# Kernel optimization log

Hardware: AMD Instinct MI355X
Metric: run time of the kernel (lower is better)

The kernel has to match this reference:

```python
import jax, jax.numpy as jnp
import numpy as np

T, B, D, H, O = 64, 64, 512, 512, 128

def setup_inputs() -> dict:
    key = jax.random.key(0)
    ks = jax.random.split(key, 8)
    s = 0.05
    return {
        "x": jax.random.normal(ks[0], (T, B, D), jnp.float32),
        "w_ih": jax.random.normal(ks[1], (T, 4 * H, D), jnp.float32) * s,
        "w_hh": jax.random.normal(ks[2], (T, 4 * H, H), jnp.float32) * s,
        "b_ih": jax.random.normal(ks[3], (T, 4 * H), jnp.float32) * s,
        "b_hh": jax.random.normal(ks[4], (T, 4 * H), jnp.float32) * s,
        "w_ho": jax.random.normal(ks[5], (O, H), jnp.float32) * s,
        "b_ho": jax.random.normal(ks[6], (O,), jnp.float32) * s,
        "lengths": jax.random.randint(ks[7], (B,), 1, T + 1, jnp.int64 if jax.config.jax_enable_x64 else jnp.int32),
    }

def _lstm_scan(x, w_ih, w_hh, b_ih, b_hh):
    bs = x.shape[1]
    h0 = jnp.zeros((bs, H), x.dtype)
    c0 = jnp.zeros((bs, H), x.dtype)

    def step(carry, inp):
        h, c = carry
        xt, Wih, Whh, bih, bhh = inp
        # gates: [B, 4H], torch gate order i, f, g, o
        gates = xt @ Wih.T + bih + h @ Whh.T + bhh
        i, f, g, o = jnp.split(gates, 4, axis=-1)
        c = jax.nn.sigmoid(f) * c + jax.nn.sigmoid(i) * jnp.tanh(g)
        h = jax.nn.sigmoid(o) * jnp.tanh(c)
        return (h, c), h

    (_, _), outs = jax.lax.scan(step, (h0, c0), (x, w_ih, w_hh, b_ih, b_hh))
    return outs  # [T, B, H]

def reference(x, w_ih, w_hh, b_ih, b_hh, w_ho, b_ho, lengths):
    outs = _lstm_scan(x, w_ih, w_hh, b_ih, b_hh)
    bs = x.shape[1]
    h_t = outs[lengths - 1, jnp.arange(bs)]  # [B, H] last valid output per seq
    logits = h_t @ w_ho.T + b_ho
    return jax.nn.log_softmax(logits, axis=1)
```

## Files before the change

### kernel.cpp

```cpp
#include <hip/hip_runtime.h>
#include <math.h>

#define TT 64
#define BB 64
#define DD 512
#define HH 512
#define G4 2048
#define OO 128

typedef unsigned short us16;
typedef __attribute__((ext_vector_type(8))) short bf16x8;
typedef __attribute__((ext_vector_type(4))) float f32x4;

__device__ __forceinline__ unsigned pk_bf16(float lo, float hi) {
  unsigned r;
  asm volatile("v_cvt_pk_bf16_f32 %0, %1, %2" : "=v"(r) : "v"(lo), "v"(hi));
  return r;
}

__device__ __forceinline__ float sigm(float v) { return 1.f / (1.f + expf(-v)); }

__device__ __forceinline__ uint4 load_b128_cc(const void* p) {
  uint4 r;
  asm volatile("global_load_dwordx4 %0, %1, off sc0 sc1" : "=v"(r) : "v"(p));
  return r;
}
__device__ __forceinline__ void store_b64_cc(void* p, uint2 v) {
  asm volatile("global_store_dwordx2 %0, %1, off sc0 sc1" ::"v"(p), "v"(v) : "memory");
}

__global__ __launch_bounds__(256) void phaseA_mfma(
    const float* __restrict__ x, const float* __restrict__ wih,
    const float* __restrict__ bih, const float* __restrict__ bhh,
    float* __restrict__ Gb) {
  __shared__ us16 xa[2][64][64];
  __shared__ us16 wbuf[2][128][64];
  const int tid = threadIdx.x;
  const int t = blockIdx.y;
  const int j0 = blockIdx.x * 128;
  const int wv = tid >> 6, lane = tid & 63;
  const int wm = wv & 1, wn = wv >> 1;
  const float* xb = x + (size_t)t * (BB * DD);
  const float* wg = wih + (size_t)t * (G4 * DD) + (size_t)j0 * DD;

  float4 xr[2][2], wr[4][2];
  int xrow[2], xc[2], wrow[4], wc[4];
#pragma unroll
  for (int i = 0; i < 2; i++) { int cid = tid + i * 256; xrow[i] = cid >> 3; xc[i] = cid & 7; }
#pragma unroll
  for (int i = 0; i < 4; i++) { int cid = tid + i * 256; wrow[i] = cid >> 3; wc[i] = cid & 7; }

  auto loadx = [&](int k0) {
#pragma unroll
    for (int i = 0; i < 2; i++) {
      const float* p = xb + xrow[i] * DD + k0 + xc[i] * 8;
      xr[i][0] = *(const float4*)p; xr[i][1] = *(const float4*)(p + 4);
    }
  };
  auto loadw = [&](int k0) {
#pragma unroll
    for (int i = 0; i < 4; i++) {
      const float* p = wg + (size_t)wrow[i] * DD + k0 + wc[i] * 8;
      wr[i][0] = *(const float4*)p; wr[i][1] = *(const float4*)(p + 4);
    }
  };
  auto store = [&](int buf) {
#pragma unroll
    for (int i = 0; i < 2; i++) {
      uint4 u;
      u.x = pk_bf16(xr[i][0].x, xr[i][0].y); u.y = pk_bf16(xr[i][0].z, xr[i][0].w);
      u.z = pk_bf16(xr[i][1].x, xr[i][1].y); u.w = pk_bf16(xr[i][1].z, xr[i][1].w);
      int p = xc[i] ^ (xrow[i] & 7);
      *(uint4*)&xa[buf][xrow[i]][p * 8] = u;
    }
#pragma unroll
    for (int i = 0; i < 4; i++) {
      uint4 u;
      u.x = pk_bf16(wr[i][0].x, wr[i][0].y); u.y = pk_bf16(wr[i][0].z, wr[i][0].w);
      u.z = pk_bf16(wr[i][1].x, wr[i][1].y); u.w = pk_bf16(wr[i][1].z, wr[i][1].w);
      int p = wc[i] ^ (wrow[i] & 7);
      *(uint4*)&wbuf[buf][wrow[i]][p * 8] = u;
    }
  };

  loadx(0); loadw(0); store(0);
  __syncthreads();

  f32x4 zero = {0.f, 0.f, 0.f, 0.f};
  f32x4 acc[2][4];
#pragma unroll
  for (int mt = 0; mt < 2; mt++)
#pragma unroll
    for (int nt = 0; nt < 4; nt++) acc[mt][nt] = zero;

  for (int s = 0; s < 8; s++) {
    const int nb = s & 1;
    if (s < 7) { loadx((s + 1) * 64); loadw((s + 1) * 64); }
#pragma unroll
    for (int ks = 0; ks < 2; ks++) {
      const int cc = ks * 4 + (lane >> 4);
      bf16x8 a[2], b[4];
#pragma unroll
      for (int mt = 0; mt < 2; mt++) {
        int r = wm * 32 + mt * 16 + (lane & 15);
        a[mt] = *(const bf16x8*)&xa[nb][r][(cc ^ (r & 7)) * 8];
      }
#pragma unroll
      for (int nt = 0; nt < 4; nt++) {
        int r = wn * 64 + nt * 16 + (lane & 15);
        b[nt] = *(const bf16x8*)&wbuf[nb][r][(cc ^ (r & 7)) * 8];
      }
#pragma unroll
      for (int mt = 0; mt < 2; mt++)
#pragma unroll
        for (int nt = 0; nt < 4; nt++)
          acc[mt][nt] = __builtin_amdgcn_mfma_f32_16x16x32_bf16(a[mt], b[nt], acc[mt][nt], 0, 0, 0);
    }
    __syncthreads();
    if (s < 7) store(nb ^ 1);
    __syncthreads();
  }

  float bias[4]; int jn[4];
#pragma unroll
  for (int nt = 0; nt < 4; nt++) {
    jn[nt] = j0 + wn * 64 + nt * 16 + (lane & 15);
    bias[nt] = bih[t * G4 + jn[nt]] + bhh[t * G4 + jn[nt]];
  }
#pragma unroll
  for (int mt = 0; mt < 2; mt++)
#pragma unroll
    for (int nt = 0; nt < 4; nt++)
#pragma unroll
      for (int e = 0; e < 4; e++) {
        int brow = wm * 32 + mt * 16 + (lane >> 4) * 4 + e;
        Gb[((size_t)t * BB + brow) * G4 + jn[nt]] = acc[mt][nt][e] + bias[nt];
      }
}

__global__ __launch_bounds__(256, 1) void lstm_persist(
    const float* __restrict__ whh, const float* __restrict__ Gb,
    const int* __restrict__ lengths, us16* __restrict__ hb,
    float* __restrict__ cbuf, float* __restrict__ hf,
    unsigned* __restrict__ flags) {
  __shared__ float gm[2][16][36];

  const int tid = threadIdx.x, bid = blockIdx.x;
  const int bh = bid & 1, ug = bid >> 1;
  const int wv = tid >> 6, lane = tid & 63;
  const int wm = wv & 1, kq = wv >> 1;
  const int l15 = lane & 15, klg = lane >> 4;

  const size_t jrow = (size_t)((l15 >> 2) * 512 + ug * 4 + (l15 & 3));

  float4 pf[8][2];
  auto prefW = [&](int tt) {
    const float* wt = whh + (size_t)tt * (G4 * HH) + jrow * HH;
#pragma unroll
    for (int s = 0; s < 8; s++) {
      const float* p = wt + (size_t)(kq * 32 + s * 4 + klg) * 8;
      pf[s][0] = *(const float4*)p;
      pf[s][1] = *(const float4*)(p + 4);
    }
  };
  bf16x8 wfrag[8];
  auto cvtW = [&]() {
#pragma unroll
    for (int s = 0; s < 8; s++) {
      uint4 u;
      u.x = pk_bf16(pf[s][0].x, pf[s][0].y); u.y = pk_bf16(pf[s][0].z, pf[s][0].w);
      u.z = pk_bf16(pf[s][1].x, pf[s][1].y); u.w = pk_bf16(pf[s][1].z, pf[s][1].w);
      wfrag[s] = __builtin_bit_cast(bf16x8, u);
    }
  };

  f32x4 gpre[4];
  auto prefG = [&](int tt) {
    if (tid < 32) {
      const float* gbp = &Gb[((size_t)tt * BB + bh * 32 + tid) * G4 + ug * 4];
#pragma unroll
      for (int q = 0; q < 4; q++) gpre[q] = *(const f32x4*)(gbp + q * 512);
    }
  };

  const int cch = ug >> 1;
  const int kqd = cch >> 5, rem = cch & 31, sd = rem >> 2, klgd = rem & 3;
  const int wmd = (tid & 31) >> 4;
  const int laned = klgd * 16 + (tid & 15);
  const int wvd = kqd * 2 + wmd;
  const size_t hst_off =
      (size_t)bh * 32768 + ((size_t)(wvd * 8 + sd) * 64 + laned) * 16 + (size_t)(ug & 1) * 8;

  const int pidx0 = (2 * lane + bh) * 4;
  const int pidx1 = (2 * (lane + 64) + bh) * 4;

  const int mylen = (tid < 32) ? lengths[bh * 32 + tid] : -2;

  prefW(0);
  prefG(0);

  for (int t = 0; t < TT; t++) {
    if (t > 0) {
      if (wv == 0) {
        const unsigned tgt = (unsigned)t;
        while (true) {
          unsigned f0 = __hip_atomic_load(&flags[pidx0], __ATOMIC_RELAXED,
                                          __HIP_MEMORY_SCOPE_AGENT);
          unsigned f1 = __hip_atomic_load(&flags[pidx1], __ATOMIC_RELAXED,
                                          __HIP_MEMORY_SCOPE_AGENT);
          if (__all(f0 >= tgt && f1 >= tgt)) break;
          __builtin_amdgcn_s_sleep(1);
        }
      }
      __syncthreads();
    }

    uint4 hfrag[8];
    {
      const char* base = (const char*)hb + (size_t)(t & 1) * 65536 + (size_t)bh * 32768 +
                         ((size_t)(wv * 8) * 64 + lane) * 16;
#pragma unroll
      for (int s = 0; s < 8; s++)
        hfrag[s] = load_b128_cc(base + (size_t)s * 1024);
    }

    cvtW();

    f32x4 gcur[4];
    if (tid < 32) {
#pragma unroll
      for (int q = 0; q < 4; q++) gcur[q] = gpre[q];
    }

    asm volatile("s_waitcnt vmcnt(0)" ::: "memory");
    __builtin_amdgcn_sched_barrier(0);

    f32x4 acc = {0.f, 0.f, 0.f, 0.f};
#pragma unroll
    for (int s = 0; s < 8; s++)
      acc = __builtin_amdgcn_mfma_f32_16x16x32_bf16(__builtin_bit_cast(bf16x8, hfrag[s]),
                                                    wfrag[s], acc, 0, 0, 0);
    *(f32x4*)&gm[kq][l15][wm * 16 + klg * 4] = acc;

    __syncthreads();

    if (tid < 32) {
      const int bg = bh * 32 + tid;
      f32x4 cv = *(const f32x4*)&cbuf[(size_t)bg * HH + ug * 4];
      float hvv[4];
#pragma unroll
      for (int u = 0; u < 4; u++) {
        float vi = gcur[0][u] + gm[0][0 + u][tid] + gm[1][0 + u][tid];
        float vf = gcur[1][u] + gm[0][4 + u][tid] + gm[1][4 + u][tid];
        float vg = gcur[2][u] + gm[0][8 + u][tid] + gm[1][8 + u][tid];
        float vo = gcur[3][u] + gm[0][12 + u][tid] + gm[1][12 + u][tid];
        float cn = sigm(vf) * cv[u] + sigm(vi) * tanhf(vg);
        cv[u] = cn;
        hvv[u] = sigm(vo) * tanhf(cn);
      }
      *(f32x4*)&cbuf[(size_t)bg * HH + ug * 4] = cv;
      uint2 hu;
      hu.x = pk_bf16(hvv[0], hvv[1]);
      hu.y = pk_bf16(hvv[2], hvv[3]);
      store_b64_cc((char*)hb + (size_t)((t + 1) & 1) * 65536 + hst_off, hu);
      if (mylen - 1 == t) {
        f32x4 hv4 = {hvv[0], hvv[1], hvv[2], hvv[3]};
        *(f32x4*)&hf[(size_t)bg * HH + ug * 4] = hv4;
      }
      asm volatile("s_waitcnt vmcnt(0)" ::: "memory");
      if (tid == 0)
        __hip_atomic_store(&flags[bid * 4], (unsigned)(t + 1), __ATOMIC_RELAXED,
                           __HIP_MEMORY_SCOPE_AGENT);
    }

    if (t + 1 < TT) { prefW(t + 1); prefG(t + 1); }
  }
}

__global__ __launch_bounds__(128) void finalK(const float* __restrict__ hf,
                                              const float* __restrict__ who,
                                              const float* __restrict__ bho,
                                              float* __restrict__ out) {
  int b = blockIdx.x, o = threadIdx.x;
  const float* h = hf + b * HH;
  const float* w = who + o * HH;
  float s = bho[o];
#pragma unroll 4
  for (int k = 0; k < HH; k += 4) {
    float4 hv = *(const float4*)(h + k);
    float4 wv = *(const float4*)(w + k);
    s += hv.x * wv.x + hv.y * wv.y + hv.z * wv.z + hv.w * wv.w;
  }
  __shared__ float red[2];
  __shared__ float red2[2];
  float m = s;
#pragma unroll
  for (int msk = 32; msk; msk >>= 1) m = fmaxf(m, __shfl_xor(m, msk));
  int wave = o >> 6;
  if ((o & 63) == 0) red[wave] = m;
  __syncthreads();
  m = fmaxf(red[0], red[1]);
  float e = expf(s - m);
#pragma unroll
  for (int msk = 32; msk; msk >>= 1) e += __shfl_xor(e, msk);
  if ((o & 63) == 0) red2[wave] = e;
  __syncthreads();
  float sum = red2[0] + red2[1];
  out[b * OO + o] = (s - m) - logf(sum);
}

extern "C" void kernel_launch(void* const* d_in, const int* in_sizes, int n_in,
                              void* d_out, int out_size, void* d_ws, size_t ws_size,
                              hipStream_t stream) {
  const float* x = (const float*)d_in[0];
  const float* wih = (const float*)d_in[1];
  const float* whh = (const float*)d_in[2];
  const float* bih = (const float*)d_in[3];
  const float* bhh = (const float*)d_in[4];
  const float* who = (const float*)d_in[5];
  const float* bho = (const float*)d_in[6];
  const int* lengths = (const int*)d_in[7];
  float* out = (float*)d_out;

  char* ws = (char*)d_ws;
  float* Gb = (float*)ws;
  us16* hb = (us16*)(ws + 33554432);
  float* cb = (float*)(ws + 33554432 + 131072);
  unsigned* flags = (unsigned*)(ws + 33554432 + 262144);
  float* hf = (float*)(ws + 33554432 + 270336);

  hipMemsetAsync(hb, 0, 270336, stream);

  phaseA_mfma<<<dim3(16, 64), 256, 0, stream>>>(x, wih, bih, bhh, Gb);
  lstm_persist<<<256, 256, 0, stream>>>(whh, Gb, lengths, hb, cb, hf, flags);
  finalK<<<BB, 128, 0, stream>>>(hf, who, bho, out);
}
```

Measured before the change: 346.4 us.

## Replace flag-based barrier with step-tagged h records and register-resident cell state

The persistent LSTM kernel stops polling per-block flag words followed by a block barrier. Each producer now writes its bf16 h values together with the step number as one 16-byte record, and consumers spin on their own loads until every record carries the expected tag, so the data doubles as the signal. The cell state stays in registers instead of a global buffer, the gate epilogue is spread over a full wave instead of 32 threads, and the next-step weight and gate prefetch is issued before the epilogue. In exchange the h buffer doubles in size with padded records, every thread performs redundant polling loads, and correctness now relies on each 16-byte store becoming visible atomically.

Measured after the change: 342.9 us. No clear change (-1.0%).

```diff
diff --git a/kernel.cpp b/kernel.cpp
--- a/kernel.cpp
+++ b/kernel.cpp
@@ -11,6 +11,7 @@
 typedef unsigned short us16;
 typedef __attribute__((ext_vector_type(8))) short bf16x8;
 typedef __attribute__((ext_vector_type(4))) float f32x4;
+typedef __attribute__((ext_vector_type(4))) unsigned u32x4;
 
 __device__ __forceinline__ unsigned pk_bf16(float lo, float hi) {
   unsigned r;
@@ -20,13 +21,13 @@
 
 __device__ __forceinline__ float sigm(float v) { return 1.f / (1.f + expf(-v)); }
 
-__device__ __forceinline__ uint4 load_b128_cc(const void* p) {
-  uint4 r;
+__device__ __forceinline__ u32x4 load_b128_cc(const void* p) {
+  u32x4 r;
   asm volatile("global_load_dwordx4 %0, %1, off sc0 sc1" : "=v"(r) : "v"(p));
   return r;
 }
-__device__ __forceinline__ void store_b64_cc(void* p, uint2 v) {
-  asm volatile("global_store_dwordx2 %0, %1, off sc0 sc1" ::"v"(p), "v"(v) : "memory");
+__device__ __forceinline__ void store_b128_cc(void* p, u32x4 v) {
+  asm volatile("global_store_dwordx4 %0, %1, off sc0 sc1" ::"v"(p), "v"(v) : "memory");
 }
 
 __global__ __launch_bounds__(256) void phaseA_mfma(
@@ -140,9 +141,8 @@
 
 __global__ __launch_bounds__(256, 1) void lstm_persist(
     const float* __restrict__ whh, const float* __restrict__ Gb,
-    const int* __restrict__ lengths, us16* __restrict__ hb,
-    float* __restrict__ cbuf, float* __restrict__ hf,
-    unsigned* __restrict__ flags) {
+    const int* __restrict__ lengths, char* __restrict__ hb,
+    float* __restrict__ hf) {
   __shared__ float gm[2][16][36];
 
   const int tid = threadIdx.x, bid = blockIdx.x;
@@ -174,106 +174,97 @@
     }
   };
 
-  f32x4 gpre[4];
+  float2 gpre[4];
   auto prefG = [&](int tt) {
-    if (tid < 32) {
-      const float* gbp = &Gb[((size_t)tt * BB + bh * 32 + tid) * G4 + ug * 4];
-#pragma unroll
-      for (int q = 0; q < 4; q++) gpre[q] = *(const f32x4*)(gbp + q * 512);
-    }
-  };
-
-  const int cch = ug >> 1;
-  const int kqd = cch >> 5, rem = cch & 31, sd = rem >> 2, klgd = rem & 3;
-  const int wmd = (tid & 31) >> 4;
-  const int laned = klgd * 16 + (tid & 15);
-  const int wvd = kqd * 2 + wmd;
-  const size_t hst_off =
-      (size_t)bh * 32768 + ((size_t)(wvd * 8 + sd) * 64 + laned) * 16 + (size_t)(ug & 1) * 8;
-
-  const int pidx0 = (2 * lane + bh) * 4;
-  const int pidx1 = (2 * (lane + 64) + bh) * 4;
-
-  const int mylen = (tid < 32) ? lengths[bh * 32 + tid] : -2;
+    if (wv == 0) {
+      const float* gbp =
+          Gb + ((size_t)tt * BB + bh * 32 + (lane & 31)) * G4 + ug * 4 + ((lane >> 5) << 1);
+#pragma unroll
+      for (int q = 0; q < 4; q++) gpre[q] = *(const float2*)(gbp + q * 512);
+    }
+  };
+
+  const size_t cbase =
+      (size_t)bh * 65536 + ((size_t)(kq * 64 + klg * 2) * 32 + wm * 16 + l15) * 16;
+  const size_t pbase = (size_t)bh * 65536 + ((size_t)ug * 32 + (lane & 31)) * 16;
+
+  const int mylen = (wv == 0) ? lengths[bh * 32 + (lane & 31)] : -2;
+  float cst[2] = {0.f, 0.f};
 
   prefW(0);
   prefG(0);
 
   for (int t = 0; t < TT; t++) {
-    if (t > 0) {
-      if (wv == 0) {
-        const unsigned tgt = (unsigned)t;
-        while (true) {
-          unsigned f0 = __hip_atomic_load(&flags[pidx0], __ATOMIC_RELAXED,
-                                          __HIP_MEMORY_SCOPE_AGENT);
-          unsigned f1 = __hip_atomic_load(&flags[pidx1], __ATOMIC_RELAXED,
-                                          __HIP_MEMORY_SCOPE_AGENT);
-          if (__all(f0 >= tgt && f1 >= tgt)) break;
-          __builtin_amdgcn_s_sleep(1);
+    cvtW();
+
+    u32x4 r0[8], r1[8];
+    if (t == 0) {
+      u32x4 z = {0u, 0u, 0u, 0u};
+#pragma unroll
+      for (int s = 0; s < 8; s++) { r0[s] = z; r1[s] = z; }
+    } else {
+      const char* sbase = hb + (size_t)(t & 1) * 131072 + cbase;
+      const unsigned tg = (unsigned)t;
+      bool ok;
+      do {
+#pragma unroll
+        for (int s = 0; s < 8; s++) {
+          r0[s] = load_b128_cc(sbase + (size_t)s * 4096);
+          r1[s] = load_b128_cc(sbase + (size_t)s * 4096 + 512);
         }
-      }
-      __syncthreads();
-    }
-
-    uint4 hfrag[8];
-    {
-      const char* base = (const char*)hb + (size_t)(t & 1) * 65536 + (size_t)bh * 32768 +
-                         ((size_t)(wv * 8) * 64 + lane) * 16;
-#pragma unroll
-      for (int s = 0; s < 8; s++)
-        hfrag[s] = load_b128_cc(base + (size_t)s * 1024);
-    }
-
-    cvtW();
-
-    f32x4 gcur[4];
-    if (tid < 32) {
+        asm volatile("s_waitcnt vmcnt(0)" ::: "memory");
+        __builtin_amdgcn_sched_barrier(0);
+        ok = true;
+#pragma unroll
+        for (int s = 0; s < 8; s++) ok = ok && (r0[s].z == tg) && (r1[s].z == tg);
+      } while (!__all(ok));
+    }
+
+    f32x4 acc = {0.f, 0.f, 0.f, 0.f};
+#pragma unroll
+    for (int s = 0; s < 8; s++) {
+      u32x4 fa;
+      fa.x = r0[s].x; fa.y = r0[s].y; fa.z = r1[s].x; fa.w = r1[s].y;
+      acc = __builtin_amdgcn_mfma_f32_16x16x32_bf16(__builtin_bit_cast(bf16x8, fa),
+                                                    wfrag[s], acc, 0, 0, 0);
+    }
+    *(f32x4*)&gm[kq][l15][wm * 16 + klg * 4] = acc;
+
+    __syncthreads();
+
+    float2 gcur[4];
+    if (wv == 0) {
 #pragma unroll
       for (int q = 0; q < 4; q++) gcur[q] = gpre[q];
     }
-
-    asm volatile("s_waitcnt vmcnt(0)" ::: "memory");
-    __builtin_amdgcn_sched_barrier(0);
-
-    f32x4 acc = {0.f, 0.f, 0.f, 0.f};
-#pragma unroll
-    for (int s = 0; s < 8; s++)
-      acc = __builtin_amdgcn_mfma_f32_16x16x32_bf16(__builtin_bit_cast(bf16x8, hfrag[s]),
-                                                    wfrag[s], acc, 0, 0, 0);
-    *(f32x4*)&gm[kq][l15][wm * 16 + klg * 4] = acc;
-
-    __syncthreads();
-
-    if (tid < 32) {
-      const int bg = bh * 32 + tid;
-      f32x4 cv = *(const f32x4*)&cbuf[(size_t)bg * HH + ug * 4];
-      float hvv[4];
-#pragma unroll
-      for (int u = 0; u < 4; u++) {
-        float vi = gcur[0][u] + gm[0][0 + u][tid] + gm[1][0 + u][tid];
-        float vf = gcur[1][u] + gm[0][4 + u][tid] + gm[1][4 + u][tid];
-        float vg = gcur[2][u] + gm[0][8 + u][tid] + gm[1][8 + u][tid];
-        float vo = gcur[3][u] + gm[0][12 + u][tid] + gm[1][12 + u][tid];
-        float cn = sigm(vf) * cv[u] + sigm(vi) * tanhf(vg);
-        cv[u] = cn;
-        hvv[u] = sigm(vo) * tanhf(cn);
-      }
-      *(f32x4*)&cbuf[(size_t)bg * HH + ug * 4] = cv;
-      uint2 hu;
-      hu.x = pk_bf16(hvv[0], hvv[1]);
-      hu.y = pk_bf16(hvv[2], hvv[3]);
-      store_b64_cc((char*)hb + (size_t)((t + 1) & 1) * 65536 + hst_off, hu);
+    if (t + 1 < TT) { prefW(t + 1); prefG(t + 1); }
+
+    if (wv == 0) {
+      const int b = lane & 31, hi = lane >> 5;
+      float hv[2];
+#pragma unroll
+      for (int uu = 0; uu < 2; uu++) {
+        const int lu = hi * 2 + uu;
+        float vi = (uu ? gcur[0].y : gcur[0].x) + gm[0][0 + lu][b] + gm[1][0 + lu][b];
+        float vf = (uu ? gcur[1].y : gcur[1].x) + gm[0][4 + lu][b] + gm[1][4 + lu][b];
+        float vg = (uu ? gcur[2].y : gcur[2].x) + gm[0][8 + lu][b] + gm[1][8 + lu][b];
+        float vo = (uu ? gcur[3].y : gcur[3].x) + gm[0][12 + lu][b] + gm[1][12 + lu][b];
+        float cn = sigm(vf) * cst[uu] + sigm(vi) * tanhf(vg);
+        cst[uu] = cn;
+        hv[uu] = sigm(vo) * tanhf(cn);
+      }
+      unsigned hw = pk_bf16(hv[0], hv[1]);
+      unsigned other = __shfl_xor(hw, 32);
       if (mylen - 1 == t) {
-        f32x4 hv4 = {hvv[0], hvv[1], hvv[2], hvv[3]};
-        *(f32x4*)&hf[(size_t)bg * HH + ug * 4] = hv4;
-      }
-      asm volatile("s_waitcnt vmcnt(0)" ::: "memory");
-      if (tid == 0)
-        __hip_atomic_store(&flags[bid * 4], (unsigned)(t + 1), __ATOMIC_RELAXED,
-                           __HIP_MEMORY_SCOPE_AGENT);
-    }
-
-    if (t + 1 < TT) { prefW(t + 1); prefG(t + 1); }
+        float2 o2; o2.x = hv[0]; o2.y = hv[1];
+        *(float2*)&hf[(size_t)(bh * 32 + b) * HH + ug * 4 + hi * 2] = o2;
+      }
+      if (hi == 0 && t + 1 < TT) {
+        u32x4 rec;
+        rec.x = hw; rec.y = other; rec.z = (unsigned)(t + 1); rec.w = 0u;
+        store_b128_cc(hb + (size_t)((t + 1) & 1) * 131072 + pbase, rec);
+      }
+    }
   }
 }
 
@@ -324,14 +315,12 @@
 
   char* ws = (char*)d_ws;
   float* Gb = (float*)ws;
-  us16* hb = (us16*)(ws + 33554432);
-  float* cb = (float*)(ws + 33554432 + 131072);
-  unsigned* flags = (unsigned*)(ws + 33554432 + 262144);
-  float* hf = (float*)(ws + 33554432 + 270336);
-
-  hipMemsetAsync(hb, 0, 270336, stream);
+  char* hb = ws + 33554432;
+  float* hf = (float*)(ws + 33554432 + 262144);
+
+  (void)hipMemsetAsync(hb, 0, 262144, stream);
 
   phaseA_mfma<<<dim3(16, 64), 256, 0, stream>>>(x, wih, bih, bhh, Gb);
-  lstm_persist<<<256, 256, 0, stream>>>(whh, Gb, lengths, hb, cb, hf, flags);
+  lstm_persist<<<256, 256, 0, stream>>>(whh, Gb, lengths, hb, hf);
   finalK<<<BB, 128, 0, stream>>>(hf, who, bho, out);
 }
```
